# Optimization experiments

Hardware: AMD Instinct MI355X
Metric: run time of the kernel (lower is better)

## Reference

```python
import jax, jax.numpy as jnp
import numpy as np


def _rope(x, C):
    # x: [B, H, W, C]; 2 spatial channel dims -> k_max = C // 4
    B, H, W, _ = x.shape
    k_max = C // 4
    theta = 1.0 / (10000.0 ** (jnp.arange(k_max, dtype=x.dtype) / k_max))
    hh, ww = jnp.meshgrid(jnp.arange(H, dtype=x.dtype), jnp.arange(W, dtype=x.dtype), indexing='ij')
    angles = jnp.concatenate([hh[..., None] * theta, ww[..., None] * theta], axis=-1)  # [H, W, C//2]
    cos, sin = jnp.cos(angles), jnp.sin(angles)
    xr = x.reshape(B, H, W, C // 2, 2)
    x_re, x_im = xr[..., 0], xr[..., 1]
    out = jnp.stack([x_re * cos - x_im * sin, x_im * cos + x_re * sin], axis=-1)
    return out.reshape(B, H, W, C)


def _forward(x, W_qk, b_qk, scale_p, dwc_w, dwc_b, img_H, img_W):
    B, N, C = x.shape
    head_dim = dwc_w.shape[0]
    h = C // head_dim
    f = 3  # focusing_factor

    qk = x @ W_qk.T + b_qk                        # [B, N, 2C]
    q, k = qk[..., :C], qk[..., C:]
    v = x

    q = _rope(q.reshape(B, img_H, img_W, C), C).reshape(B, N, C)
    k = _rope(k.reshape(B, img_H, img_W, C), C).reshape(B, N, C)

    q = jax.nn.elu(q) + 1.0
    k = jax.nn.elu(k) + 1.0

    scale = jax.nn.softplus(scale_p)              # [1, 1, C]
    q = q / scale
    k = k / scale

    q_norm = jnp.linalg.norm(q, axis=-1, keepdims=True)
    k_norm = jnp.linalg.norm(k, axis=-1, keepdims=True)
    q = q ** f
    k = k ** f
    q = q / jnp.linalg.norm(q, axis=-1, keepdims=True) * q_norm
    k = k / jnp.linalg.norm(k, axis=-1, keepdims=True) * k_norm

    q = q.reshape(B, N, h, head_dim).transpose(0, 2, 1, 3)   # [B, h, N, d]
    k = k.reshape(B, N, h, head_dim).transpose(0, 2, 1, 3)
    v = v.reshape(B, N, h, head_dim).transpose(0, 2, 1, 3)

    k_mean = k.mean(axis=2, keepdims=True)                    # [B, h, 1, d]
    z = 1.0 / (jnp.einsum('bhnd,bhmd->bhnm', q, k_mean) + 1e-6)  # [B, h, N, 1]

    s = float(N) ** (-0.5)
    kv = jnp.einsum('bhnd,bhne->bhde', k * s, v * s)          # [B, h, d, d]
    out = jnp.einsum('bhnd,bhde->bhne', q, kv) * z            # [B, h, N, d]
    out = out.transpose(0, 2, 1, 3).reshape(B, N, C)

    # depthwise conv residual on v
    v_img = v.reshape(B * h, img_H, img_W, head_dim).transpose(0, 3, 1, 2)  # [B*h, d, H, W]
    conv = jax.lax.conv_general_dilated(
        v_img, dwc_w, window_strides=(1, 1), padding='SAME',
        dimension_numbers=('NCHW', 'OIHW', 'NCHW'),
        feature_group_count=head_dim) + dwc_b[None, :, None, None]
    out = out + conv.reshape(B, C, N).transpose(0, 2, 1)
    return out


def setup_inputs() -> dict:
    key = jax.random.key(0)
    ks = jax.random.split(key, 6)
    B, img_H, img_W, C, head_dim, ksz = 8, 64, 64, 512, 32, 5
    N = img_H * img_W
    x = jax.random.normal(ks[0], (B, N, C), dtype=jnp.float32)
    W_qk = jax.random.normal(ks[1], (2 * C, C), dtype=jnp.float32) * 0.02
    b_qk = jnp.zeros((2 * C,), dtype=jnp.float32)
    scale_p = jax.random.normal(ks[2], (1, 1, C), dtype=jnp.float32) * 0.02
    fan_out = ksz * ksz  # depthwise: out_channels/groups = 1
    dwc_w = jax.random.normal(ks[3], (head_dim, 1, ksz, ksz), dtype=jnp.float32) * np.sqrt(2.0 / fan_out)
    dwc_b = jnp.zeros((head_dim,), dtype=jnp.float32)
    return {"x": x, "W_qk": W_qk, "b_qk": b_qk, "scale_p": scale_p,
            "dwc_w": dwc_w, "dwc_b": dwc_b, "img_H": img_H, "img_W": img_W}


def reference(x, W_qk, b_qk, scale_p, dwc_w, dwc_b, img_H, img_W):
    return _forward(x, W_qk, b_qk, scale_p, dwc_w, dwc_b, img_H, img_W)
```

## Files before the change

### kernel.cpp

```cpp
#include <hip/hip_runtime.h>
#include <math.h>

#define B_SZ 8
#define IMG_H 64
#define IMG_W 64
#define N_TOK 4096
#define C_DIM 512
#define HEADS 16
#define HDIM 32
#define M_ROWS (B_SZ * N_TOK)
#define QK_COLS (2 * C_DIM)

#define THETA_COEF (-0.07195578415606394f)

typedef __attribute__((ext_vector_type(8))) __bf16 bf16x8;
typedef __attribute__((ext_vector_type(4))) float f32x4;

__device__ __forceinline__ void async_ld16(void* lds, const void* g) {
    __builtin_amdgcn_global_load_lds(
        (const __attribute__((address_space(1))) unsigned*)g,
        (__attribute__((address_space(3))) unsigned*)lds, 16, 0, 0);
}

__device__ __forceinline__ unsigned short f2bf(float f) {
    unsigned u = __float_as_uint(f);
    u += 0x7FFF + ((u >> 16) & 1);
    return (unsigned short)(u >> 16);
}

__global__ __launch_bounds__(256) void prep_kernel(
    const float* __restrict__ x, const float* __restrict__ Wqk,
    const float* __restrict__ scale_p,
    unsigned short* __restrict__ xb, unsigned short* __restrict__ Wb,
    float* __restrict__ lut)
{
    int bid = blockIdx.x;
    int t = threadIdx.x;
    if (bid < 16384) {
        int i = bid * 256 + t;
        float4 v = ((const float4*)x)[i];
        ushort4 o;
        o.x = f2bf(v.x); o.y = f2bf(v.y); o.z = f2bf(v.z); o.w = f2bf(v.w);
        ((ushort4*)xb)[i] = o;
    } else if (bid < 16896) {
        int i = (bid - 16384) * 256 + t;
        float4 v = ((const float4*)Wqk)[i];
        ushort4 o;
        o.x = f2bf(v.x); o.y = f2bf(v.y); o.z = f2bf(v.z); o.w = f2bf(v.w);
        ((ushort4*)Wb)[i] = o;
    } else {
        int idx = (bid - 16896) * 256 + t;
        int pos = idx >> 7, tt = idx & 127;
        float theta = expf((float)tt * THETA_COEF);
        float ang = (float)pos * theta;
        lut[idx] = cosf(ang);
        lut[idx + 8192] = sinf(ang);
        if (idx < 512) lut[16384 + idx] = 1.0f / log1pf(expf(scale_p[idx]));
    }
}

#define GBM 128
#define GBN 128
#define GBK 32

#define EPI_I(I, ACC) do {                                                    \
    float cr = cI, sr = sI;                                                   \
    _Pragma("unroll")                                                         \
    for (int r = 0; r < 4; ++r) {                                             \
        int m = m0 + wm + (I) * 16 + quad * 4 + r;                            \
        float val = (ACC)[r] + bias;                                          \
        float oth = __shfl_xor(val, 1);                                       \
        float rot = is_im ? (val * cr + oth * sr) : (val * cr - oth * sr);    \
        rot = (rot > 0.f) ? (rot + 1.f) : __expf(rot);                        \
        dst[(size_t)m * C_DIM + ch] = rot * rspv;                             \
        float tc = cr * c1 - sr * s1, ts = sr * c1 + cr * s1;                 \
        cr = tc; sr = ts;                                                     \
    }                                                                         \
    float uc = cI * c16 - sI * s16, us = sI * c16 + cI * s16;                 \
    cI = uc; sI = us;                                                         \
} while (0)

#define EPI_J(J, A0, A1, A2, A3) do {                                         \
    int c = n0 + wn + (J) * 16 + l16;                                         \
    int ch = c & 511;                                                         \
    float bias = bqk[c];                                                      \
    float rspv = rsp[ch];                                                     \
    int tt = ch >> 1;                                                         \
    int tl = tt & 127;                                                        \
    float cI, sI, c1, s1, c16, s16;                                           \
    if (tt < 128) {               \
        int pos = ((m0 + wm) & (N_TOK - 1)) >> 6;                             \
        cI = lut[pos * 128 + tl]; sI = lut[pos * 128 + tl + 8192];            \
        c1 = 1.f; s1 = 0.f; c16 = 1.f; s16 = 0.f;                             \
    } else {                  \
        int pos0 = quad * 4;                                                  \
        cI = lut[pos0 * 128 + tl]; sI = lut[pos0 * 128 + tl + 8192];          \
        c1  = lut[128 + tl];       s1  = lut[128 + tl + 8192];                \
        c16 = lut[2048 + tl];      s16 = lut[2048 + tl + 8192];               \
    }                                                                         \
    float* dst = (c < C_DIM) ? qW : kW;                                       \
    EPI_I(0, A0); EPI_I(1, A1); EPI_I(2, A2); EPI_I(3, A3);                   \
} while (0)

__global__ __launch_bounds__(256, 1) void gemm_mfma_kernel(
    const unsigned short* __restrict__ xb,
    const unsigned short* __restrict__ Wb,
    const float* __restrict__ bqk,
    const float* __restrict__ lut,
    float* __restrict__ qW,
    float* __restrict__ kW)
{
    __shared__ char lds[32768];

    const float* rsp = lut + 16384;

    const int t = threadIdx.x;
    const int wave = t >> 6;
    const int lane = t & 63;
    const int quad = lane >> 4;
    const int l16 = lane & 15;
    const int is_im = l16 & 1;

    const int flat = blockIdx.x + 8 * blockIdx.y;
    const int xcd = flat & 7;
    const int ii_ = flat >> 3;
    const int n0 = (ii_ & 7) * GBN;
    const int m0 = (xcd * 32 + (ii_ >> 3)) * GBM;

    const int wm = (wave >> 1) * 64;
    const int wn = (wave & 1) * 64;

    const int srow = t >> 2;
    const int sj = t & 3;

    f32x4 acc00 = {0.f,0.f,0.f,0.f}, acc01 = {0.f,0.f,0.f,0.f},
          acc02 = {0.f,0.f,0.f,0.f}, acc03 = {0.f,0.f,0.f,0.f},
          acc10 = {0.f,0.f,0.f,0.f}, acc11 = {0.f,0.f,0.f,0.f},
          acc12 = {0.f,0.f,0.f,0.f}, acc13 = {0.f,0.f,0.f,0.f},
          acc20 = {0.f,0.f,0.f,0.f}, acc21 = {0.f,0.f,0.f,0.f},
          acc22 = {0.f,0.f,0.f,0.f}, acc23 = {0.f,0.f,0.f,0.f},
          acc30 = {0.f,0.f,0.f,0.f}, acc31 = {0.f,0.f,0.f,0.f},
          acc32 = {0.f,0.f,0.f,0.f}, acc33 = {0.f,0.f,0.f,0.f};

    const int swz = (l16 >> 1) & 3;
    const int co = (quad ^ swz) * 16;

    auto stage = [&](int k0, int b) {
#pragma unroll
        for (int p = 0; p < 2; ++p) {
            int m = p * 64 + srow;
            int jp = sj ^ ((m >> 1) & 3);
            const unsigned short* ga = xb + (size_t)(m0 + m) * C_DIM + k0 + jp * 8;
            async_ld16(lds + b * 16384 + p * 4096 + wave * 1024, ga);
            const unsigned short* gb = Wb + (size_t)(n0 + m) * C_DIM + k0 + jp * 8;
            async_ld16(lds + b * 16384 + 8192 + p * 4096 + wave * 1024, gb);
        }
    };

    stage(0, 0);
    __syncthreads();
    int buf = 0;

    for (int k0 = 0; k0 < C_DIM; k0 += GBK) {
        if (k0 + GBK < C_DIM) stage(k0 + GBK, buf ^ 1);

        const char* As = lds + buf * 16384;
        const char* Bs = As + 8192;
        bf16x8 a0 = *(const bf16x8*)(As + (wm + 0 * 16 + l16) * 64 + co);
        bf16x8 a1 = *(const bf16x8*)(As + (wm + 1 * 16 + l16) * 64 + co);
        bf16x8 a2 = *(const bf16x8*)(As + (wm + 2 * 16 + l16) * 64 + co);
        bf16x8 a3 = *(const bf16x8*)(As + (wm + 3 * 16 + l16) * 64 + co);
        bf16x8 b0 = *(const bf16x8*)(Bs + (wn + 0 * 16 + l16) * 64 + co);
        bf16x8 b1 = *(const bf16x8*)(Bs + (wn + 1 * 16 + l16) * 64 + co);
        bf16x8 b2 = *(const bf16x8*)(Bs + (wn + 2 * 16 + l16) * 64 + co);
        bf16x8 b3 = *(const bf16x8*)(Bs + (wn + 3 * 16 + l16) * 64 + co);

        acc00 = __builtin_amdgcn_mfma_f32_16x16x32_bf16(a0, b0, acc00, 0, 0, 0);
        acc01 = __builtin_amdgcn_mfma_f32_16x16x32_bf16(a0, b1, acc01, 0, 0, 0);
        acc02 = __builtin_amdgcn_mfma_f32_16x16x32_bf16(a0, b2, acc02, 0, 0, 0);
        acc03 = __builtin_amdgcn_mfma_f32_16x16x32_bf16(a0, b3, acc03, 0, 0, 0);
        acc10 = __builtin_amdgcn_mfma_f32_16x16x32_bf16(a1, b0, acc10, 0, 0, 0);
        acc11 = __builtin_amdgcn_mfma_f32_16x16x32_bf16(a1, b1, acc11, 0, 0, 0);
        acc12 = __builtin_amdgcn_mfma_f32_16x16x32_bf16(a1, b2, acc12, 0, 0, 0);
        acc13 = __builtin_amdgcn_mfma_f32_16x16x32_bf16(a1, b3, acc13, 0, 0, 0);
        acc20 = __builtin_amdgcn_mfma_f32_16x16x32_bf16(a2, b0, acc20, 0, 0, 0);
        acc21 = __builtin_amdgcn_mfma_f32_16x16x32_bf16(a2, b1, acc21, 0, 0, 0);
        acc22 = __builtin_amdgcn_mfma_f32_16x16x32_bf16(a2, b2, acc22, 0, 0, 0);
        acc23 = __builtin_amdgcn_mfma_f32_16x16x32_bf16(a2, b3, acc23, 0, 0, 0);
        acc30 = __builtin_amdgcn_mfma_f32_16x16x32_bf16(a3, b0, acc30, 0, 0, 0);
        acc31 = __builtin_amdgcn_mfma_f32_16x16x32_bf16(a3, b1, acc31, 0, 0, 0);
        acc32 = __builtin_amdgcn_mfma_f32_16x16x32_bf16(a3, b2, acc32, 0, 0, 0);
        acc33 = __builtin_amdgcn_mfma_f32_16x16x32_bf16(a3, b3, acc33, 0, 0, 0);

        __syncthreads();
        buf ^= 1;
    }

    EPI_J(0, acc00, acc10, acc20, acc30);
    EPI_J(1, acc01, acc11, acc21, acc31);
    EPI_J(2, acc02, acc12, acc22, acc32);
    EPI_J(3, acc03, acc13, acc23, acc33);
}

__global__ __launch_bounds__(256) void norm_kernel(
    const float* __restrict__ qW, const float* __restrict__ kW,
    float* __restrict__ sq, float* __restrict__ sk)
{
    int wave = threadIdx.x >> 6;
    int lane = threadIdx.x & 63;
    int m = blockIdx.x * 4 + wave;
    const float4* qr = (const float4*)(qW + (size_t)m * C_DIM);
    const float4* kr = (const float4*)(kW + (size_t)m * C_DIM);
    float q2 = 0.f, q6 = 0.f, k2 = 0.f, k6 = 0.f;
#pragma unroll
    for (int l = 0; l < 2; ++l) {
        float4 q4 = qr[lane + l * 64];
        float4 k4 = kr[lane + l * 64];
        float qq;
        qq = q4.x * q4.x; q2 += qq; q6 += qq * qq * qq;
        qq = q4.y * q4.y; q2 += qq; q6 += qq * qq * qq;
        qq = q4.z * q4.z; q2 += qq; q6 += qq * qq * qq;
        qq = q4.w * q4.w; q2 += qq; q6 += qq * qq * qq;
        qq = k4.x * k4.x; k2 += qq; k6 += qq * qq * qq;
        qq = k4.y * k4.y; k2 += qq; k6 += qq * qq * qq;
        qq = k4.z * k4.z; k2 += qq; k6 += qq * qq * qq;
        qq = k4.w * k4.w; k2 += qq; k6 += qq * qq * qq;
    }
#pragma unroll
    for (int off = 32; off > 0; off >>= 1) {
        q2 += __shfl_down(q2, off);
        q6 += __shfl_down(q6, off);
        k2 += __shfl_down(k2, off);
        k6 += __shfl_down(k6, off);
    }
    if (lane == 0) {
        sq[m] = sqrtf(q2) / sqrtf(q6);
        sk[m] = sqrtf(k2) / sqrtf(k6);
    }
}

#define NSPLIT 8
#define ROWS_PER_SPLIT (N_TOK / NSPLIT)

__global__ __launch_bounds__(256) void kv_partial_kernel(
    const float* __restrict__ x, const float* __restrict__ kW,
    const float* __restrict__ sk,
    float* __restrict__ kvp, float* __restrict__ kmp)
{
    int g = blockIdx.x >> 3;
    int split = blockIdx.x & 7;
    int b = g >> 4, h = g & 15;
    int n_start = split * ROWS_PER_SPLIT;

    __shared__ float smem[5120];
    float* kf = smem;
    float* vv = smem + 64 * 36;

    int t = threadIdx.x;
    int wave = t >> 6, lane = t & 63;
    int srow = t >> 3;
    int scol = (t & 7) * 4;
    int d0 = (lane >> 3) * 4;
    int e0 = (lane & 7) * 4;

    float acc[4][4] = {{0.f}};
    float4 kmacc = make_float4(0.f, 0.f, 0.f, 0.f);

    float4 kreg[2], vreg[2];
    float sreg[2];
#pragma unroll
    for (int h2 = 0; h2 < 2; ++h2) {
        int n = n_start + h2 * 32 + srow;
        size_t base = ((size_t)(b * N_TOK + n)) * C_DIM + h * HDIM + scol;
        kreg[h2] = *(const float4*)&kW[base];
        vreg[h2] = *(const float4*)&x[base];
        sreg[h2] = sk[b * N_TOK + n];
    }

    for (int tt = 0; tt < ROWS_PER_SPLIT / 64; ++tt) {
        __syncthreads();
#pragma unroll
        for (int h2 = 0; h2 < 2; ++h2) {
            int row = h2 * 32 + srow;
            float4 k4 = kreg[h2];
            float s = sreg[h2];
            float4 k3;
            k3.x = k4.x * k4.x * k4.x * s;
            k3.y = k4.y * k4.y * k4.y * s;
            k3.z = k4.z * k4.z * k4.z * s;
            k3.w = k4.w * k4.w * k4.w * s;
            *(float4*)&kf[row * 36 + scol] = k3;
            *(float4*)&vv[row * 36 + scol] = vreg[h2];
            kmacc.x += k3.x; kmacc.y += k3.y;
            kmacc.z += k3.z; kmacc.w += k3.w;
        }
        if (tt < ROWS_PER_SPLIT / 64 - 1) {
            int nb = n_start + (tt + 1) * 64;
#pragma unroll
            for (int h2 = 0; h2 < 2; ++h2) {
                int n = nb + h2 * 32 + srow;
                size_t base = ((size_t)(b * N_TOK + n)) * C_DIM + h * HDIM + scol;
                kreg[h2] = *(const float4*)&kW[base];
                vreg[h2] = *(const float4*)&x[base];
                sreg[h2] = sk[b * N_TOK + n];
            }
        }
        __syncthreads();

        const float* kfp = kf + (wave * 16) * 36 + d0;
        const float* vvp = vv + (wave * 16) * 36 + e0;
#pragma unroll
        for (int nn = 0; nn < 16; ++nn) {
            float4 k4 = *(const float4*)(kfp + nn * 36);
            float4 v4 = *(const float4*)(vvp + nn * 36);
            acc[0][0] += k4.x * v4.x; acc[0][1] += k4.x * v4.y;
            acc[0][2] += k4.x * v4.z; acc[0][3] += k4.x * v4.w;
            acc[1][0] += k4.y * v4.x; acc[1][1] += k4.y * v4.y;
            acc[1][2] += k4.y * v4.z; acc[1][3] += k4.y * v4.w;
            acc[2][0] += k4.z * v4.x; acc[2][1] += k4.z * v4.y;
            acc[2][2] += k4.z * v4.z; acc[2][3] += k4.z * v4.w;
            acc[3][0] += k4.w * v4.x; acc[3][1] += k4.w * v4.y;
            acc[3][2] += k4.w * v4.z; acc[3][3] += k4.w * v4.w;
        }
    }

    __syncthreads();
    float* red = smem;
    float* kmr = smem + 4096;
#pragma unroll
    for (int di = 0; di < 4; ++di) {
        float4 v = make_float4(acc[di][0], acc[di][1], acc[di][2], acc[di][3]);
        *(float4*)&red[wave * 1024 + (d0 + di) * 32 + e0] = v;
    }
    *(float4*)&kmr[srow * 32 + scol] = kmacc;
    __syncthreads();

    size_t pbase = (size_t)blockIdx.x * 1024;
    for (int idx = t; idx < 1024; idx += 256) {
        float s = red[idx] + red[1024 + idx] + red[2048 + idx] + red[3072 + idx];
        kvp[pbase + idx] = s;
    }
    if (t < 32) {
        float s = 0.f;
#pragma unroll
        for (int r = 0; r < 32; ++r) s += kmr[r * 32 + t];
        kmp[blockIdx.x * 32 + t] = s;
    }
}

__global__ __launch_bounds__(256) void kv_reduce_kernel(
    const float* __restrict__ kvp, const float* __restrict__ kmp,
    float* __restrict__ kv, float* __restrict__ km)
{
    int g = blockIdx.x;
    int t = threadIdx.x;
    for (int idx = t; idx < 1024; idx += 256) {
        float s = 0.f;
#pragma unroll
        for (int sp = 0; sp < NSPLIT; ++sp)
            s += kvp[((size_t)(g * NSPLIT + sp)) * 1024 + idx];
        int d = idx >> 5, e = idx & 31;
        kv[(size_t)g * 1024 + e * 32 + d] = s * (1.0f / 4096.0f);
    }
    if (t < 32) {
        float s = 0.f;
#pragma unroll
        for (int sp = 0; sp < NSPLIT; ++sp) s += kmp[(g * NSPLIT + sp) * 32 + t];
        km[g * 32 + t] = s * (1.0f / 4096.0f);
    }
}

__global__ __launch_bounds__(256) void attn_conv_kernel(
    const float* __restrict__ qW, const float* __restrict__ sq,
    const float* __restrict__ kvT, const float* __restrict__ km,
    const float* __restrict__ x, const float* __restrict__ w,
    const float* __restrict__ wbias, float* __restrict__ out)
{
    int g = blockIdx.x;
    int b = g >> 4, h = g & 15;
    int n0 = blockIdx.y * 128;

    __shared__ float qf[16][36];
    __shared__ float ob[128][34];
    __shared__ float wl[25][32];

    int t = threadIdx.x;
    for (int idx = t; idx < 800; idx += 256) {
        int o = idx & 31, tap = idx >> 5;
        wl[tap][o] = w[o * 25 + tap];
    }

    int e = t & 15;
    int nl = t >> 4;
    int sd = e * 2;

    const float* kvg = kvT + (size_t)g * 1024;
    float4 kva[8], kvb[8], kmr[8];
#pragma unroll
    for (int j = 0; j < 8; ++j) {
        kva[j] = *(const float4*)&kvg[e * 32 + j * 4];
        kvb[j] = *(const float4*)&kvg[(e + 16) * 32 + j * 4];
        kmr[j] = *(const float4*)&km[g * 32 + j * 4];
    }

    size_t rbase = ((size_t)(b * N_TOK + n0 + nl)) * C_DIM + h * HDIM;

    float2 q2 = *(const float2*)&qW[rbase + sd];
    float sv = sq[b * N_TOK + n0 + nl];

    for (int ch = 0; ch < 8; ++ch) {
        __syncthreads();
        *(float2*)&qf[nl][sd] =
            make_float2(q2.x * q2.x * q2.x * sv, q2.y * q2.y * q2.y * sv);

        float2 q2n; float svn;
        if (ch < 7) {
            size_t nb = rbase + (size_t)(ch + 1) * 16 * C_DIM;
            q2n = *(const float2*)&qW[nb + sd];
            svn = sq[b * N_TOK + n0 + (ch + 1) * 16 + nl];
        }
        __syncthreads();

        float s1a = 0.f, s1b = 0.f, s2 = 0.f;
#pragma unroll
        for (int j = 0; j < 8; ++j) {
            float4 q4 = *(const float4*)&qf[nl][j * 4];
            s1a += q4.x * kva[j].x + q4.y * kva[j].y
                 + q4.z * kva[j].z + q4.w * kva[j].w;
            s1b += q4.x * kvb[j].x + q4.y * kvb[j].y
                 + q4.z * kvb[j].z + q4.w * kvb[j].w;
            s2  += q4.x * kmr[j].x + q4.y * kmr[j].y
                 + q4.z * kmr[j].z + q4.w * kmr[j].w;
        }
        float z = 1.0f / (s2 + 1e-6f);
        ob[ch * 16 + nl][e] = s1a * z;
        ob[ch * 16 + nl][e + 16] = s1b * z;

        if (ch < 7) { q2 = q2n; sv = svn; }
    }

    __syncthreads();

    int r = t >> 7;
    int jg = (t >> 3) & 15;
    int cg = t & 7;
    int j0 = jg * 4;
    int o4 = cg * 4;
    int i = (n0 >> 6) + r;

    const float* xbase = x + ((size_t)b * N_TOK) * C_DIM + h * HDIM + o4;

    float4 b4 = *(const float4*)&wbias[o4];
    float4 acc[4] = {b4, b4, b4, b4};

#pragma unroll
    for (int ki = 0; ki < 5; ++ki) {
        int ii = i + ki - 2;
        if (ii < 0 || ii >= IMG_H) continue;
        const float* xr = xbase + (size_t)ii * 64 * C_DIM;
        float4 row[8];
#pragma unroll
        for (int jx = 0; jx < 8; ++jx) {
            int jj = j0 + jx - 2;
            row[jx] = (jj >= 0 && jj < IMG_W)
                          ? *(const float4*)(xr + (size_t)jj * C_DIM)
                          : make_float4(0.f, 0.f, 0.f, 0.f);
        }
#pragma unroll
        for (int kj = 0; kj < 5; ++kj) {
            float4 w4 = *(const float4*)&wl[ki * 5 + kj][o4];
#pragma unroll
            for (int jo = 0; jo < 4; ++jo) {
                acc[jo].x += w4.x * row[jo + kj].x;
                acc[jo].y += w4.y * row[jo + kj].y;
                acc[jo].z += w4.z * row[jo + kj].z;
                acc[jo].w += w4.w * row[jo + kj].w;
            }
        }
    }

    float* op = out + ((size_t)(b * N_TOK + i * 64 + j0)) * C_DIM + h * HDIM + o4;
#pragma unroll
    for (int jo = 0; jo < 4; ++jo) {
        float4 a = *(const float4*)&ob[r * 64 + j0 + jo][o4];
        acc[jo].x += a.x;
        acc[jo].y += a.y;
        acc[jo].z += a.z;
        acc[jo].w += a.w;
        *(float4*)(op + (size_t)jo * C_DIM) = acc[jo];
    }
}

extern "C" void kernel_launch(void* const* d_in, const int* in_sizes, int n_in,
                              void* d_out, int out_size, void* d_ws, size_t ws_size,
                              hipStream_t stream) {
    const float* x       = (const float*)d_in[0];
    const float* Wqk     = (const float*)d_in[1];
    const float* bqk     = (const float*)d_in[2];
    const float* scale_p = (const float*)d_in[3];
    const float* dwc_w   = (const float*)d_in[4];
    const float* dwc_b   = (const float*)d_in[5];
    float* out = (float*)d_out;
    float* ws = (float*)d_ws;

    float* qW  = ws;
    float* sq  = qW + (size_t)M_ROWS * C_DIM;
    float* sk  = sq + M_ROWS;
    float* kvp = sk + M_ROWS;
    float* kmp = kvp + (size_t)1024 * 1024;
    float* kv  = kmp + 1024 * 32;
    float* km  = kv + 128 * 1024;
    unsigned short* xb = (unsigned short*)(km + 2048);
    unsigned short* Wb = xb + (size_t)M_ROWS * C_DIM;
    float* lut = (float*)(Wb + (size_t)QK_COLS * C_DIM);
    float* kW  = out;

    prep_kernel<<<16928, 256, 0, stream>>>(x, Wqk, scale_p, xb, Wb, lut);

    dim3 gg(QK_COLS / GBN, M_ROWS / GBM);
    gemm_mfma_kernel<<<gg, 256, 0, stream>>>(xb, Wb, bqk, lut, qW, kW);

    norm_kernel<<<M_ROWS / 4, 256, 0, stream>>>(qW, kW, sq, sk);

    kv_partial_kernel<<<128 * NSPLIT, 256, 0, stream>>>(x, kW, sk, kvp, kmp);
    kv_reduce_kernel<<<128, 256, 0, stream>>>(kvp, kmp, kv, km);

    dim3 g4(128, 32);
    attn_conv_kernel<<<g4, 256, 0, stream>>>(qW, sq, kv, km, x, dwc_w, dwc_b, out);
}
```

Before: 320.5 us.

## Fuse row-norm partial sums into GEMM epilogue and software-pipeline conv row loads

The GEMM epilogue now accumulates per-row sums of squares and sixth powers for q and k, reduces them across lanes, and writes per-column-tile partials into a scratch buffer. A small finishing kernel sums the 8 partials per row, replacing the norm kernel that re-read both 64 MB q/k buffers. Separately, the depthwise conv loop is rewritten with two row buffers so the next row's loads are issued before the current row is computed. The trade-off is extra epilogue register pressure and shuffles in the GEMM, and the partials reuse the kvp workspace, which is fine because kv_partial runs only after norm_fin.

```diff
diff --git a/kernel.cpp b/kernel.cpp
--- a/kernel.cpp
+++ b/kernel.cpp
@@ -63,7 +63,7 @@
 #define GBN 128
 #define GBK 32
 
-#define EPI_I(I, ACC) do {                                                    \
+#define EPI_I(I, ACC, N2, N6) do {                                            \
     float cr = cI, sr = sI;                                                   \
     _Pragma("unroll")                                                         \
     for (int r = 0; r < 4; ++r) {                                             \
@@ -72,7 +72,11 @@
         float oth = __shfl_xor(val, 1);                                       \
         float rot = is_im ? (val * cr + oth * sr) : (val * cr - oth * sr);    \
         rot = (rot > 0.f) ? (rot + 1.f) : __expf(rot);                        \
-        dst[(size_t)m * C_DIM + ch] = rot * rspv;                             \
+        float ov = rot * rspv;                                                \
+        dst[(size_t)m * C_DIM + ch] = ov;                                     \
+        float ox = ov * ov;                                                   \
+        (N2)[r] += ox;                                                        \
+        (N6)[r] += ox * ox * ox;                                              \
         float tc = cr * c1 - sr * s1, ts = sr * c1 + cr * s1;                 \
         cr = tc; sr = ts;                                                     \
     }                                                                         \
@@ -99,7 +103,26 @@
         c16 = lut[2048 + tl];      s16 = lut[2048 + tl + 8192];               \
     }                                                                         \
     float* dst = (c < C_DIM) ? qW : kW;                                       \
-    EPI_I(0, A0); EPI_I(1, A1); EPI_I(2, A2); EPI_I(3, A3);                   \
+    EPI_I(0, A0, n2_0, n6_0); EPI_I(1, A1, n2_1, n6_1);                       \
+    EPI_I(2, A2, n2_2, n6_2); EPI_I(3, A3, n2_3, n6_3);                       \
+} while (0)
+
+#define NRED(I, N2, N6) do {                                                  \
+    f32x4 v2s, v6s;                                                           \
+    _Pragma("unroll")                                                         \
+    for (int r = 0; r < 4; ++r) {                                             \
+        float a2 = (N2)[r], a6 = (N6)[r];                                     \
+        a2 += __shfl_xor(a2, 1); a6 += __shfl_xor(a6, 1);                     \
+        a2 += __shfl_xor(a2, 2); a6 += __shfl_xor(a6, 2);                     \
+        a2 += __shfl_xor(a2, 4); a6 += __shfl_xor(a6, 4);                     \
+        a2 += __shfl_xor(a2, 8); a6 += __shfl_xor(a6, 8);                     \
+        v2s[r] = a2; v6s[r] = a6;                                             \
+    }                                                                         \
+    if (l16 == 0) {                                                           \
+        int m = m0 + wm + (I) * 16 + quad * 4;                                \
+        *(float4*)&np2[pslot * 32768 + m] = *(float4*)&v2s;                   \
+        *(float4*)&np6[pslot * 32768 + m] = *(float4*)&v6s;                   \
+    }                                                                         \
 } while (0)
 
 __global__ __launch_bounds__(256, 1) void gemm_mfma_kernel(
@@ -108,7 +131,8 @@
     const float* __restrict__ bqk,
     const float* __restrict__ lut,
     float* __restrict__ qW,
-    float* __restrict__ kW)
+    float* __restrict__ kW,
+    float* __restrict__ nrmP)
 {
     __shared__ char lds[32768];
 
@@ -196,47 +220,39 @@
         buf ^= 1;
     }
 
+    f32x4 n2_0 = {0.f,0.f,0.f,0.f}, n2_1 = {0.f,0.f,0.f,0.f},
+          n2_2 = {0.f,0.f,0.f,0.f}, n2_3 = {0.f,0.f,0.f,0.f},
+          n6_0 = {0.f,0.f,0.f,0.f}, n6_1 = {0.f,0.f,0.f,0.f},
+          n6_2 = {0.f,0.f,0.f,0.f}, n6_3 = {0.f,0.f,0.f,0.f};
+
     EPI_J(0, acc00, acc10, acc20, acc30);
     EPI_J(1, acc01, acc11, acc21, acc31);
     EPI_J(2, acc02, acc12, acc22, acc32);
     EPI_J(3, acc03, acc13, acc23, acc33);
-}
-
-__global__ __launch_bounds__(256) void norm_kernel(
-    const float* __restrict__ qW, const float* __restrict__ kW,
-    float* __restrict__ sq, float* __restrict__ sk)
+
+    const int pslot = ((n0 >> 7) & 3) * 2 + (wn >> 6);
+    float* np2 = nrmP + ((n0 < C_DIM) ? 0 : 524288);
+    float* np6 = np2 + 262144;
+    NRED(0, n2_0, n6_0);
+    NRED(1, n2_1, n6_1);
+    NRED(2, n2_2, n6_2);
+    NRED(3, n2_3, n6_3);
+}
+
+__global__ __launch_bounds__(256) void norm_fin_kernel(
+    const float* __restrict__ nrmP, float* __restrict__ sq, float* __restrict__ sk)
 {
-    int wave = threadIdx.x >> 6;
-    int lane = threadIdx.x & 63;
-    int m = blockIdx.x * 4 + wave;
-    const float4* qr = (const float4*)(qW + (size_t)m * C_DIM);
-    const float4* kr = (const float4*)(kW + (size_t)m * C_DIM);
+    int m = blockIdx.x * 256 + threadIdx.x;
     float q2 = 0.f, q6 = 0.f, k2 = 0.f, k6 = 0.f;
 #pragma unroll
-    for (int l = 0; l < 2; ++l) {
-        float4 q4 = qr[lane + l * 64];
-        float4 k4 = kr[lane + l * 64];
-        float qq;
-        qq = q4.x * q4.x; q2 += qq; q6 += qq * qq * qq;
-        qq = q4.y * q4.y; q2 += qq; q6 += qq * qq * qq;
-        qq = q4.z * q4.z; q2 += qq; q6 += qq * qq * qq;
-        qq = q4.w * q4.w; q2 += qq; q6 += qq * qq * qq;
-        qq = k4.x * k4.x; k2 += qq; k6 += qq * qq * qq;
-        qq = k4.y * k4.y; k2 += qq; k6 += qq * qq * qq;
-        qq = k4.z * k4.z; k2 += qq; k6 += qq * qq * qq;
-        qq = k4.w * k4.w; k2 += qq; k6 += qq * qq * qq;
-    }
-#pragma unroll
-    for (int off = 32; off > 0; off >>= 1) {
-        q2 += __shfl_down(q2, off);
-        q6 += __shfl_down(q6, off);
-        k2 += __shfl_down(k2, off);
-        k6 += __shfl_down(k6, off);
-    }
-    if (lane == 0) {
-        sq[m] = sqrtf(q2) / sqrtf(q6);
-        sk[m] = sqrtf(k2) / sqrtf(k6);
-    }
+    for (int p = 0; p < 8; ++p) {
+        q2 += nrmP[p * 32768 + m];
+        q6 += nrmP[262144 + p * 32768 + m];
+        k2 += nrmP[524288 + p * 32768 + m];
+        k6 += nrmP[786432 + p * 32768 + m];
+    }
+    sq[m] = sqrtf(q2) / sqrtf(q6);
+    sk[m] = sqrtf(k2) / sqrtf(k6);
 }
 
 #define NSPLIT 8
@@ -370,6 +386,38 @@
     }
 }
 
+#define LOADROW(KI, ROW) do {                                                 \
+    int ii = i + (KI) - 2;                                                    \
+    if (ii >= 0 && ii < IMG_H) {                                              \
+        const float* xr = xbase + (size_t)ii * 64 * C_DIM;                    \
+        _Pragma("unroll")                                                     \
+        for (int jx = 0; jx < 8; ++jx) {                                      \
+            int jj = j0 + jx - 2;                                             \
+            ROW[jx] = (jj >= 0 && jj < IMG_W)                                 \
+                          ? *(const float4*)(xr + (size_t)jj * C_DIM)         \
+                          : make_float4(0.f, 0.f, 0.f, 0.f);                  \
+        }                                                                     \
+    } else {                                                                  \
+        _Pragma("unroll")                                                     \
+        for (int jx = 0; jx < 8; ++jx)                                        \
+            ROW[jx] = make_float4(0.f, 0.f, 0.f, 0.f);                        \
+    }                                                                         \
+} while (0)
+
+#define COMPROW(KI, ROW) do {                                                 \
+    _Pragma("unroll")                                                         \
+    for (int kj = 0; kj < 5; ++kj) {                                          \
+        float4 w4 = *(const float4*)&wl[(KI) * 5 + kj][o4];                   \
+        _Pragma("unroll")                                                     \
+        for (int jo = 0; jo < 4; ++jo) {                                      \
+            acc[jo].x += w4.x * ROW[jo + kj].x;                               \
+            acc[jo].y += w4.y * ROW[jo + kj].y;                               \
+            acc[jo].z += w4.z * ROW[jo + kj].z;                               \
+            acc[jo].w += w4.w * ROW[jo + kj].w;                               \
+        }                                                                     \
+    }                                                                         \
+} while (0)
+
 __global__ __launch_bounds__(256) void attn_conv_kernel(
     const float* __restrict__ qW, const float* __restrict__ sq,
     const float* __restrict__ kvT, const float* __restrict__ km,
@@ -453,31 +501,14 @@
     float4 b4 = *(const float4*)&wbias[o4];
     float4 acc[4] = {b4, b4, b4, b4};
 
-#pragma unroll
-    for (int ki = 0; ki < 5; ++ki) {
-        int ii = i + ki - 2;
-        if (ii < 0 || ii >= IMG_H) continue;
-        const float* xr = xbase + (size_t)ii * 64 * C_DIM;
-        float4 row[8];
-#pragma unroll
-        for (int jx = 0; jx < 8; ++jx) {
-            int jj = j0 + jx - 2;
-            row[jx] = (jj >= 0 && jj < IMG_W)
-                          ? *(const float4*)(xr + (size_t)jj * C_DIM)
-                          : make_float4(0.f, 0.f, 0.f, 0.f);
-        }
-#pragma unroll
-        for (int kj = 0; kj < 5; ++kj) {
-            float4 w4 = *(const float4*)&wl[ki * 5 + kj][o4];
-#pragma unroll
-            for (int jo = 0; jo < 4; ++jo) {
-                acc[jo].x += w4.x * row[jo + kj].x;
-                acc[jo].y += w4.y * row[jo + kj].y;
-                acc[jo].z += w4.z * row[jo + kj].z;
-                acc[jo].w += w4.w * row[jo + kj].w;
-            }
-        }
-    }
+    float4 rowA[8], rowB[8];
+    LOADROW(0, rowA);
+    LOADROW(1, rowB);
+    COMPROW(0, rowA); LOADROW(2, rowA);
+    COMPROW(1, rowB); LOADROW(3, rowB);
+    COMPROW(2, rowA); LOADROW(4, rowA);
+    COMPROW(3, rowB);
+    COMPROW(4, rowA);
 
     float* op = out + ((size_t)(b * N_TOK + i * 64 + j0)) * C_DIM + h * HDIM + o4;
 #pragma unroll
@@ -514,13 +545,14 @@
     unsigned short* Wb = xb + (size_t)M_ROWS * C_DIM;
     float* lut = (float*)(Wb + (size_t)QK_COLS * C_DIM);
     float* kW  = out;
+    float* nrmP = kvp;
 
     prep_kernel<<<16928, 256, 0, stream>>>(x, Wqk, scale_p, xb, Wb, lut);
 
     dim3 gg(QK_COLS / GBN, M_ROWS / GBM);
-    gemm_mfma_kernel<<<gg, 256, 0, stream>>>(xb, Wb, bqk, lut, qW, kW);
-
-    norm_kernel<<<M_ROWS / 4, 256, 0, stream>>>(qW, kW, sq, sk);
+    gemm_mfma_kernel<<<gg, 256, 0, stream>>>(xb, Wb, bqk, lut, qW, kW, nrmP);
+
+    norm_fin_kernel<<<128, 256, 0, stream>>>(nrmP, sq, sk);
 
     kv_partial_kernel<<<128 * NSPLIT, 256, 0, stream>>>(x, kW, sk, kvp, kmp);
     kv_reduce_kernel<<<128, 256, 0, stream>>>(kvp, kmp, kv, km);
```

Measured after the change: 336.6 us. 5.0% more time.
